# Kernel optimization log

Hardware: AMD Instinct MI355X
Metric: run time of the kernel (lower is better)

Reference implementation:

```python
import jax, jax.numpy as jnp
import numpy as np

B = 4096      # batch
D = 256       # flattened input feature dim
NUMFEAT = 1 + D + D * (D + 1) // 2  # 33153: bias + linear + quadratic terms


def setup_inputs() -> dict:
    key = jax.random.key(0)
    k1, k2 = jax.random.split(key)
    x = jax.random.normal(k1, (B, D), dtype=jnp.float32)
    # nn.Linear(numfeat, 10, bias=False): weight shape (10, numfeat)
    W = jax.random.normal(k2, (10, NUMFEAT), dtype=jnp.float32) * 0.01
    return {"x": x, "W": W}


def reference(x, W):
    # x: (B, D) -- original does x.view(B, -1); already 2D here.
    b, d = x.shape
    # sklearn PolynomialFeatures(degree=2) column order:
    # [1, x_0..x_{d-1}, x_0*x_0, x_0*x_1, ..., x_{d-1}*x_{d-1}]
    # i.e. combinations_with_replacement == upper-triangular (incl. diagonal)
    iu0, iu1 = np.triu_indices(d)  # static index constants
    ones = jnp.ones((b, 1), dtype=x.dtype)
    cross = x[:, iu0] * x[:, iu1]          # (B, D*(D+1)/2)
    feats = jnp.concatenate([ones, x, cross], axis=1)  # (B, NUMFEAT)
    return feats @ W.T                      # (B, 10)
```

## Files before the change

kernel.cpp:

```cpp
#include <hip/hip_runtime.h>


#define DD 256
#define NF 33153
#define BM 64
#define TPB 256
#define ASTRIDE 264

typedef __attribute__((ext_vector_type(8))) short short8;
typedef __attribute__((ext_vector_type(4))) float floatx4;

__device__ inline unsigned short f2bf(float f) {
    unsigned u = __builtin_bit_cast(unsigned, f);
    return (unsigned short)((u + 0x7FFFu + ((u >> 16) & 1u)) >> 16);
}

__global__ __launch_bounds__(TPB)
void gbuild_kernel(const float* __restrict__ W, unsigned short* __restrict__ G) {
    int oi = blockIdx.x;
    int o = oi >> 8, i = oi & 255;
    int j = threadIdx.x;
    int base = o * NF + 257 + i * DD - (i * (i - 1)) / 2 - i;
    float v = (j >= i) ? W[base + j] : 0.f;
    G[oi * DD + j] = f2bf(v);
}

__global__ __launch_bounds__(TPB, 3)
void PolynomialRegression_75385265979710_kernel(const float* __restrict__ x,
                                                const float* __restrict__ W,
                                                const unsigned short* __restrict__ G,
                                                float* __restrict__ out) {
    __shared__ __align__(16) unsigned short As[BM * ASTRIDE];
    __shared__ float red[4 * BM];

    const int tid  = threadIdx.x;
    const int lane = tid & 63;
    const int wave = tid >> 6;
    const int ln   = lane & 15;
    const int quad = lane >> 4;
    const int rowbase = blockIdx.x * BM;
    const int o   = blockIdx.y;
    const int wn0 = wave * 64;

#pragma unroll
    for (int it = 0; it < 8; ++it) {
        int idx = it * 2048 + tid * 8;
        int r = idx >> 8, c = idx & 255;
        float4 v0 = *(const float4*)&x[(rowbase + r) * DD + c];
        float4 v1 = *(const float4*)&x[(rowbase + r) * DD + c + 4];
        short8 p;
        p[0] = (short)f2bf(v0.x); p[1] = (short)f2bf(v0.y);
        p[2] = (short)f2bf(v0.z); p[3] = (short)f2bf(v0.w);
        p[4] = (short)f2bf(v1.x); p[5] = (short)f2bf(v1.y);
        p[6] = (short)f2bf(v1.z); p[7] = (short)f2bf(v1.w);
        *(short8*)&As[r * ASTRIDE + c] = p;
    }
    __syncthreads();

    floatx4 acc[4][4];
#pragma unroll
    for (int mt = 0; mt < 4; ++mt)
#pragma unroll
        for (int nt = 0; nt < 4; ++nt) acc[mt][nt] = (floatx4)0.f;

    const unsigned short* bp[4];
#pragma unroll
    for (int t = 0; t < 4; ++t)
        bp[t] = G + (o * DD + wn0 + t * 16 + ln) * DD + quad * 8;

#pragma unroll
    for (int kt = 0; kt < 4; ++kt) {
        if (kt >= wave) {
#pragma unroll
            for (int ks = 0; ks < 2; ++ks) {
                const int kk = kt * 64 + ks * 32;
                short8 a[4], b[4];
#pragma unroll
                for (int nt = 0; nt < 4; ++nt)
                    b[nt] = *(const short8*)(bp[nt] + kk);
#pragma unroll
                for (int mt = 0; mt < 4; ++mt)
                    a[mt] = *(const short8*)&As[(mt * 16 + ln) * ASTRIDE + kk + quad * 8];
#pragma unroll
                for (int mt = 0; mt < 4; ++mt)
#pragma unroll
                    for (int nt = 0; nt < 4; ++nt)
                        acc[mt][nt] = __builtin_amdgcn_mfma_f32_16x16x32_bf16(
                            a[mt], b[nt], acc[mt][nt], 0, 0, 0);
            }
        }
    }

    float w1[4];
#pragma unroll
    for (int nt = 0; nt < 4; ++nt)
        w1[nt] = W[o * NF + 1 + wn0 + nt * 16 + ln];

#pragma unroll
    for (int mt = 0; mt < 4; ++mt) {
#pragma unroll
        for (int r = 0; r < 4; ++r) {
            const int m = mt * 16 + quad * 4 + r;
            float p = 0.f;
#pragma unroll
            for (int nt = 0; nt < 4; ++nt) {
                float xv = x[(rowbase + m) * DD + wn0 + nt * 16 + ln];
                p = fmaf(xv, acc[mt][nt][r] + w1[nt], p);
            }
            p += __shfl_xor(p, 1);
            p += __shfl_xor(p, 2);
            p += __shfl_xor(p, 4);
            p += __shfl_xor(p, 8);
            if (ln == 0) red[wave * BM + m] = p;
        }
    }
    __syncthreads();

    if (tid < BM) {
        const int m = tid;
        float s = red[m] + red[BM + m] + red[2 * BM + m] + red[3 * BM + m] + W[o * NF];
        out[(rowbase + m) * 10 + o] = s;
    }
}

extern "C" void kernel_launch(void* const* d_in, const int* in_sizes, int n_in,
                              void* d_out, int out_size, void* d_ws, size_t ws_size,
                              hipStream_t stream) {
    const float* x = (const float*)d_in[0];
    const float* W = (const float*)d_in[1];
    float* out = (float*)d_out;

    unsigned short* G = (unsigned short*)d_ws;

    gbuild_kernel<<<10 * DD, TPB, 0, stream>>>(W, G);

    dim3 grid(4096 / BM, 10);
    PolynomialRegression_75385265979710_kernel<<<grid, TPB, 0, stream>>>(x, W, G, out);
}
```

Measured before the change: 73.58 us.

## Read packed triangular W directly in GEMM, drop G prebuild, balance triangle across waves

Removes the separate kernel that expanded the upper-triangular weights into a dense bf16 matrix G. The main kernel now loads W rows straight from their packed triangular offsets and converts them to bf16 in registers, masking only the diagonal blocks. Rows are assigned to waves in complementary 32-row groups (g and 7-g) so every wave does the same amount of triangle work, where before it was uneven. It also uses a cheaper perm-based bf16 pack with plain round-half-up. The costs are an unaligned fp32 global read of W that is twice as wide as the old bf16 read, plus a runtime-bounded loop.

```diff
diff --git a/kernel.cpp b/kernel.cpp
--- a/kernel.cpp
+++ b/kernel.cpp
@@ -3,59 +3,58 @@
 
 #define DD 256
 #define NF 33153
-#define BM 64
 #define TPB 256
 #define ASTRIDE 264
 
 typedef __attribute__((ext_vector_type(8))) short short8;
 typedef __attribute__((ext_vector_type(4))) float floatx4;
+typedef __attribute__((ext_vector_type(4), aligned(4))) float float4a;
 
-__device__ inline unsigned short f2bf(float f) {
-    unsigned u = __builtin_bit_cast(unsigned, f);
-    return (unsigned short)((u + 0x7FFFu + ((u >> 16) & 1u)) >> 16);
+union S8U { unsigned u[4]; short8 s; };
+
+__device__ inline unsigned pack2(float lo, float hi) {
+    unsigned a = __builtin_bit_cast(unsigned, hi) + 0x8000u;
+    unsigned b = __builtin_bit_cast(unsigned, lo) + 0x8000u;
+    return __builtin_amdgcn_perm(a, b, 0x07060302u);
 }
 
 __global__ __launch_bounds__(TPB)
-void gbuild_kernel(const float* __restrict__ W, unsigned short* __restrict__ G) {
-    int oi = blockIdx.x;
-    int o = oi >> 8, i = oi & 255;
-    int j = threadIdx.x;
-    int base = o * NF + 257 + i * DD - (i * (i - 1)) / 2 - i;
-    float v = (j >= i) ? W[base + j] : 0.f;
-    G[oi * DD + j] = f2bf(v);
-}
-
-__global__ __launch_bounds__(TPB, 3)
 void PolynomialRegression_75385265979710_kernel(const float* __restrict__ x,
                                                 const float* __restrict__ W,
-                                                const unsigned short* __restrict__ G,
                                                 float* __restrict__ out) {
-    __shared__ __align__(16) unsigned short As[BM * ASTRIDE];
-    __shared__ float red[4 * BM];
+    __shared__ __align__(16) unsigned short As[64 * ASTRIDE];
+    __shared__ float red[4 * 64];
 
     const int tid  = threadIdx.x;
-    const int lane = tid & 63;
-    const int wave = tid >> 6;
-    const int ln   = lane & 15;
-    const int quad = lane >> 4;
-    const int rowbase = blockIdx.x * BM;
-    const int o   = blockIdx.y;
-    const int wn0 = wave * 64;
+    const int lane = tid & 63, wave = tid >> 6;
+    const int ln   = lane & 15, quad = lane >> 4;
+    const int q8   = quad * 8;
+    const int rowbase = blockIdx.x * 64;
+    const int o  = blockIdx.y;
+    const int g1 = wave, g2 = 7 - wave;
 
 #pragma unroll
     for (int it = 0; it < 8; ++it) {
         int idx = it * 2048 + tid * 8;
         int r = idx >> 8, c = idx & 255;
-        float4 v0 = *(const float4*)&x[(rowbase + r) * DD + c];
-        float4 v1 = *(const float4*)&x[(rowbase + r) * DD + c + 4];
-        short8 p;
-        p[0] = (short)f2bf(v0.x); p[1] = (short)f2bf(v0.y);
-        p[2] = (short)f2bf(v0.z); p[3] = (short)f2bf(v0.w);
-        p[4] = (short)f2bf(v1.x); p[5] = (short)f2bf(v1.y);
-        p[6] = (short)f2bf(v1.z); p[7] = (short)f2bf(v1.w);
-        *(short8*)&As[r * ASTRIDE + c] = p;
+        const float* src = &x[(rowbase + r) * DD + c];
+        float4a v0 = *(const float4a*)src;
+        float4a v1 = *(const float4a*)(src + 4);
+        S8U p;
+        p.u[0] = pack2(v0.x, v0.y); p.u[1] = pack2(v0.z, v0.w);
+        p.u[2] = pack2(v1.x, v1.y); p.u[3] = pack2(v1.z, v1.w);
+        *(short8*)&As[r * ASTRIDE + c] = p.s;
     }
     __syncthreads();
+
+    int iRow[4], bBase[4];
+#pragma unroll
+    for (int nt = 0; nt < 4; ++nt) {
+        int g = (nt < 2) ? g1 : g2;
+        int i = g * 32 + (nt & 1) * 16 + ln;
+        iRow[nt]  = i;
+        bBase[nt] = o * NF + 257 + i * 255 - ((i * (i - 1)) >> 1);
+    }
 
     floatx4 acc[4][4];
 #pragma unroll
@@ -63,38 +62,65 @@
 #pragma unroll
         for (int nt = 0; nt < 4; ++nt) acc[mt][nt] = (floatx4)0.f;
 
-    const unsigned short* bp[4];
+    auto loadA = [&](int kk, short8* a) {
 #pragma unroll
-    for (int t = 0; t < 4; ++t)
-        bp[t] = G + (o * DD + wn0 + t * 16 + ln) * DD + quad * 8;
+        for (int mt = 0; mt < 4; ++mt)
+            a[mt] = *(const short8*)&As[(mt * 16 + ln) * ASTRIDE + kk + q8];
+    };
+    auto loadB = [&](int nt, int kk) -> short8 {
+        const float* p = &W[bBase[nt] + kk + q8];
+        float4a w0 = *(const float4a*)p;
+        float4a w1 = *(const float4a*)(p + 4);
+        S8U r;
+        r.u[0] = pack2(w0.x, w0.y); r.u[1] = pack2(w0.z, w0.w);
+        r.u[2] = pack2(w1.x, w1.y); r.u[3] = pack2(w1.z, w1.w);
+        return r.s;
+    };
+    auto loadBmask = [&](int nt, int kk) -> short8 {
+        int di = iRow[nt] - kk;
+        const float* p = &W[bBase[nt] + kk + q8];
+        float4a w0 = *(const float4a*)p;
+        float4a w1 = *(const float4a*)(p + 4);
+        float f[8] = {w0.x, w0.y, w0.z, w0.w, w1.x, w1.y, w1.z, w1.w};
+#pragma unroll
+        for (int e = 0; e < 8; ++e)
+            if (q8 + e < di) f[e] = 0.f;
+        S8U r;
+        r.u[0] = pack2(f[0], f[1]); r.u[1] = pack2(f[2], f[3]);
+        r.u[2] = pack2(f[4], f[5]); r.u[3] = pack2(f[6], f[7]);
+        return r.s;
+    };
+    auto mfma2 = [&](short8* a, short8 b0, short8 b1, int nlo) {
+#pragma unroll
+        for (int mt = 0; mt < 4; ++mt) {
+            acc[mt][nlo]     = __builtin_amdgcn_mfma_f32_16x16x32_bf16(a[mt], b0, acc[mt][nlo],     0, 0, 0);
+            acc[mt][nlo + 1] = __builtin_amdgcn_mfma_f32_16x16x32_bf16(a[mt], b1, acc[mt][nlo + 1], 0, 0, 0);
+        }
+    };
 
-#pragma unroll
-    for (int kt = 0; kt < 4; ++kt) {
-        if (kt >= wave) {
-#pragma unroll
-            for (int ks = 0; ks < 2; ++ks) {
-                const int kk = kt * 64 + ks * 32;
-                short8 a[4], b[4];
-#pragma unroll
-                for (int nt = 0; nt < 4; ++nt)
-                    b[nt] = *(const short8*)(bp[nt] + kk);
-#pragma unroll
-                for (int mt = 0; mt < 4; ++mt)
-                    a[mt] = *(const short8*)&As[(mt * 16 + ln) * ASTRIDE + kk + quad * 8];
-#pragma unroll
-                for (int mt = 0; mt < 4; ++mt)
-#pragma unroll
-                    for (int nt = 0; nt < 4; ++nt)
-                        acc[mt][nt] = __builtin_amdgcn_mfma_f32_16x16x32_bf16(
-                            a[mt], b[nt], acc[mt][nt], 0, 0, 0);
-            }
-        }
+    {
+        short8 a[4];
+        loadA(g1 * 32, a);
+        mfma2(a, loadBmask(0, g1 * 32), loadBmask(1, g1 * 32), 0);
+        loadA(g2 * 32, a);
+        mfma2(a, loadBmask(2, g2 * 32), loadBmask(3, g2 * 32), 2);
+    }
+    for (int c = g1 + 1; c <= g2; ++c) {
+        short8 a[4];
+        loadA(c * 32, a);
+        mfma2(a, loadB(0, c * 32), loadB(1, c * 32), 0);
+    }
+    for (int c = g2 + 1; c < 8; ++c) {
+        short8 a[4];
+        loadA(c * 32, a);
+        mfma2(a, loadB(0, c * 32), loadB(1, c * 32), 0);
+        mfma2(a, loadB(2, c * 32), loadB(3, c * 32), 2);
     }
 
-    float w1[4];
+    float w1v[4];
 #pragma unroll
     for (int nt = 0; nt < 4; ++nt)
-        w1[nt] = W[o * NF + 1 + wn0 + nt * 16 + ln];
+        w1v[nt] = W[o * NF + 1 + iRow[nt]];
 
 #pragma unroll
     for (int mt = 0; mt < 4; ++mt) {
@@ -104,22 +130,21 @@
             float p = 0.f;
 #pragma unroll
             for (int nt = 0; nt < 4; ++nt) {
-                float xv = x[(rowbase + m) * DD + wn0 + nt * 16 + ln];
-                p = fmaf(xv, acc[mt][nt][r] + w1[nt], p);
+                float xv = x[(rowbase + m) * DD + iRow[nt]];
+                p = fmaf(xv, acc[mt][nt][r] + w1v[nt], p);
             }
             p += __shfl_xor(p, 1);
             p += __shfl_xor(p, 2);
             p += __shfl_xor(p, 4);
             p += __shfl_xor(p, 8);
-            if (ln == 0) red[wave * BM + m] = p;
+            if (ln == 0) red[wave * 64 + m] = p;
         }
     }
     __syncthreads();
 
-    if (tid < BM) {
-        const int m = tid;
-        float s = red[m] + red[BM + m] + red[2 * BM + m] + red[3 * BM + m] + W[o * NF];
-        out[(rowbase + m) * 10 + o] = s;
+    if (tid < 64) {
+        float s = red[tid] + red[64 + tid] + red[128 + tid] + red[192 + tid] + W[o * NF];
+        out[(rowbase + tid) * 10 + o] = s;
     }
 }
 
@@ -130,10 +155,6 @@
     const float* W = (const float*)d_in[1];
     float* out = (float*)d_out;
 
-    unsigned short* G = (unsigned short*)d_ws;
-
-    gbuild_kernel<<<10 * DD, TPB, 0, stream>>>(W, G);
-
-    dim3 grid(4096 / BM, 10);
-    PolynomialRegression_75385265979710_kernel<<<grid, TPB, 0, stream>>>(x, W, G, out);
+    dim3 grid(4096 / 64, 10);
+    PolynomialRegression_75385265979710_kernel<<<grid, TPB, 0, stream>>>(x, W, out);
 }
```

Result: faster. 71.65 us (-2.6%).
